# Optimization experiments

Hardware: AMD Instinct MI355X
Metric: run time of the kernel (lower is better)

The kernel has to match this reference:

```python
import jax, jax.numpy as jnp
import numpy as np
import math

D_MODEL = 256
PRED_LEN = 256
K = 32
LOW_FREQ = 1


def setup_inputs() -> dict:
    key = jax.random.key(0)
    x = jax.random.normal(key, (8, 1024, D_MODEL), dtype=jnp.float32)
    return {"x": x}


def reference(x):
    """x: (b, t, d) -> reconstructed/extrapolated series (b, t+pred_len, d)."""
    b, t, d = x.shape
    k_ = K  # K < t//2, so the explicit-k branch of the torch module is taken

    x_freq = jnp.fft.rfft(x, axis=1)  # (b, t//2+1, d) complex
    if t % 2 == 0:
        x_freq_high = x_freq[:, LOW_FREQ:-1]  # drop DC..low_freq-1 and Nyquist
    else:
        x_freq_high = x_freq[:, LOW_FREQ:]

    # top-k magnitudes over the frequency axis, independently per (b, d)
    mag = jnp.abs(x_freq_high)                                   # (b, F, d)
    _, idx = jax.lax.top_k(jnp.transpose(mag, (0, 2, 1)), k_)    # (b, d, k)
    idx = jnp.transpose(idx, (0, 2, 1)) + LOW_FREQ               # (b, k, d) into x_freq

    x_freq_topk = jnp.take_along_axis(x_freq, idx, axis=1)       # (b, k, d) complex
    freqs = jnp.fft.rfftfreq(t).astype(x.dtype)                  # (t//2+1,)
    f_topk = freqs[idx]                                          # (b, k, d)

    # append conjugate / negative-frequency pair for a real reconstruction
    x_ext = jnp.concatenate([x_freq_topk, jnp.conj(x_freq_topk)], axis=1)  # (b, 2k, d)
    f_ext = jnp.concatenate([f_topk, -f_topk], axis=1)                     # (b, 2k, d)

    t_val = jnp.arange(t + PRED_LEN, dtype=x.dtype)              # (T,)
    amp = (jnp.abs(x_ext) / t)[:, :, None, :]                    # (b, 2k, 1, d)
    phase = jnp.angle(x_ext)[:, :, None, :]                      # (b, 2k, 1, d)
    arg = (2.0 * math.pi) * f_ext[:, :, None, :] * t_val[None, None, :, None] + phase
    x_time = amp * jnp.cos(arg)                                  # (b, 2k, T, d)
    return jnp.sum(x_time, axis=1)                               # (b, T, d)
```

## Files before the change

### kernel.cpp

```cpp
#include <hip/hip_runtime.h>
#include <math.h>

#define T_LEN 1024
#define PRED_LEN 256
#define OUT_T (T_LEN + PRED_LEN)
#define DM 256
#define KSEL 32

#define TWO_PI_F 6.2831853071795864769f
#define INV1024  0.0009765625f
#define RTAU 1e-4f

#define SPAD(i) ((i) + ((i) >> 5))

__device__ __constant__ float W16RF[16] = {
    1.0f,  0.92387953f,  0.70710678f,  0.38268343f, 0.0f, -0.38268343f, -0.70710678f, -0.92387953f,
   -1.0f, -0.92387953f, -0.70710678f, -0.38268343f, 0.0f,  0.38268343f,  0.70710678f,  0.92387953f };
__device__ __constant__ float W16IF[16] = {
    0.0f, -0.38268343f, -0.70710678f, -0.92387953f, -1.0f, -0.92387953f, -0.70710678f, -0.38268343f,
    0.0f,  0.38268343f,  0.70710678f,  0.92387953f,  1.0f,  0.92387953f,  0.70710678f,  0.38268343f };

#define R2_ 0.70710678118654752440f
__device__ __constant__ float CW8[8] = { 1.0f,  R2_, 0.0f, -R2_, -1.0f, -R2_,  0.0f,  R2_ };
__device__ __constant__ float SW8[8] = { 0.0f,  R2_, 1.0f,  R2_,  0.0f, -R2_, -1.0f, -R2_ };

__global__ void fl_twiddle_kernel(double* __restrict__ gwr, double* __restrict__ gwi,
                                  float* __restrict__ gwrF, float* __restrict__ gwiF) {
    int e = blockIdx.x * 64 + threadIdx.x;
    double ang = (double)e * (6.283185307179586476925286766559 / 1024.0);
    double c = cos(ang), s = -sin(ang);
    gwr[e] = c; gwi[e] = s;
    gwrF[e] = (float)c; gwiF[e] = (float)s;
}

__global__ void __launch_bounds__(256, 4)
fl_fused_kernel(const float* __restrict__ x,
                const double* __restrict__ gwr, const double* __restrict__ gwi,
                const float* __restrict__ gwrF, const float* __restrict__ gwiF,
                float* __restrict__ out) {
    __shared__ float gspR[SPAD(1023) + 1], gspI[SPAD(1023) + 1];
    __shared__ float2 xsh[1024];
    __shared__ float mg[1024];
    __shared__ int hist[512];
    __shared__ int   selMs[2 * KSEL];
    __shared__ float selAs[2 * KSEL], selBs[2 * KSEL];

    const int tid  = threadIdx.x;
    const int lane = tid & 63;
    const int w    = tid >> 6;

    const int bid = blockIdx.x;
    const int sp  = ((bid & 7) << 7) | (bid >> 3);
    const int b   = sp >> 7;
    const int d0  = (sp & 127) << 1;

    for (int j = 0; j < 4; ++j) {
        int e = tid + (j << 8);
        gspR[SPAD(e)] = gwrF[e];
        gspI[SPAD(e)] = gwiF[e];
        xsh[e] = *reinterpret_cast<const float2*>(&x[(((size_t)(b << 10) + e) << 8) + d0]);
    }
    __syncthreads();

    float Fr[4][4], Fi[4][4];
#pragma unroll
    for (int n1a = 0; n1a < 4; ++n1a) {
        float2 a  = xsh[lane + 64 * (n1a + 0)];
        float2 bb = xsh[lane + 64 * (n1a + 4)];
        float2 cV = xsh[lane + 64 * (n1a + 8)];
        float2 d  = xsh[lane + 64 * (n1a + 12)];
        float t0r = a.x + cV.x, t0i = a.y + cV.y;
        float t1r = a.x - cV.x, t1i = a.y - cV.y;
        float t2r = bb.x + d.x, t2i = bb.y + d.y;
        float t3r = bb.x - d.x, t3i = bb.y - d.y;
        Fr[n1a][0] = t0r + t2r;  Fi[n1a][0] = t0i + t2i;
        Fr[n1a][2] = t0r - t2r;  Fi[n1a][2] = t0i - t2i;
        Fr[n1a][1] = t1r + t3i;  Fi[n1a][1] = t1i - t3r;
        Fr[n1a][3] = t1r - t3i;  Fi[n1a][3] = t1i + t3r;
    }

    float ar[4], ai[4];
#pragma unroll
    for (int q = 0; q < 4; ++q) {
        const int k1 = (w << 2) | q;
        float cr = Fr[0][q], ci = Fi[0][q];
#pragma unroll
        for (int n1a = 1; n1a < 4; ++n1a) {
            int e = (n1a * k1) & 15;
            float wr = W16RF[e], wi = W16IF[e];
            cr += Fr[n1a][q] * wr - Fi[n1a][q] * wi;
            ci += Fr[n1a][q] * wi + Fi[n1a][q] * wr;
        }
        int et = (lane * k1) & 1023;
        float twr = gspR[SPAD(et)], twi = gspI[SPAD(et)];
        ar[q] = cr * twr - ci * twi;
        ai[q] = cr * twi + ci * twr;
    }

#pragma unroll
    for (int s = 0; s < 6; ++s) {
        const int half = 32 >> s;
        const int e = (lane & (half - 1)) << s;
        const float wr = gspR[SPAD(e << 4)];
        const float wi = gspI[SPAD(e << 4)];
        const bool up = (lane & half) != 0;
#pragma unroll
        for (int q = 0; q < 4; ++q) {
            float orr = __shfl_xor(ar[q], half);
            float oii = __shfl_xor(ai[q], half);
            float sr = ar[q] + orr, si = ai[q] + oii;
            float dr = orr - ar[q], di = oii - ai[q];
            float ur = dr * wr - di * wi;
            float ui = dr * wi + di * wr;
            ar[q] = up ? ur : sr;
            ai[q] = up ? ui : si;
        }
    }
    __syncthreads();

    {
        const int krev = (int)(__brev((unsigned)lane) >> 26);
#pragma unroll
        for (int q = 0; q < 4; ++q) {
            int k = ((w << 2) | q) + (krev << 4);
            gspR[SPAD(k)] = ar[q];
            gspI[SPAD(k)] = ai[q];
        }
    }
    __syncthreads();

#pragma unroll
    for (int h = 0; h < 2; ++h) {
        int m = tid + (h << 8);
        int n = (1024 - m) & 1023;
        float rm = gspR[SPAD(m)], iv = gspI[SPAD(m)];
        float rn = gspR[SPAD(n)], in_ = gspI[SPAD(n)];
        float rr0 = 0.5f * (rm + rn),  ii0 = 0.5f * (iv - in_);
        float rr1 = 0.5f * (iv + in_), ii1 = 0.5f * (rn - rm);
        mg[m]       = rr0 * rr0 + ii0 * ii0;
        mg[512 + m] = rr1 * rr1 + ii1 * ii1;
    }
    __syncthreads();

    if (tid < 128) {
        const int c = tid >> 6;
        const float* mgc = mg + (c << 9);
        int* histc = hist + (c << 8);

        float v[8]; int hiw[8];
#pragma unroll
        for (int q = 0; q < 8; ++q) v[q] = mgc[(q << 6) | lane];
        if (lane == 0) v[0] = -1.0f;
#pragma unroll
        for (int q = 0; q < 8; ++q) hiw[q] = __float_as_int(v[q]);

        int mx = hiw[0];
#pragma unroll
        for (int q = 1; q < 8; ++q) mx = max(mx, hiw[q]);
#pragma unroll
        for (int off = 1; off < 64; off <<= 1) mx = max(mx, __shfl_xor(mx, off));

        const int base = (mx >> 20) - 250;
        int idx[8];
#pragma unroll
        for (int q = 0; q < 8; ++q) {
            int t = (hiw[q] >> 20) - base;
            idx[q] = t < 0 ? 0 : t;
        }

        *reinterpret_cast<int4*>(&histc[lane << 2]) = int4{0, 0, 0, 0};
#pragma unroll
        for (int q = 0; q < 8; ++q) atomicAdd(&histc[idx[q]], 1);

        int4 cc = *reinterpret_cast<int4*>(&histc[lane << 2]);
        int s_local = cc.x + cc.y + cc.z + cc.w;

        int s = s_local;
#pragma unroll
        for (int off = 1; off < 64; off <<= 1) {
            int t = __shfl_down(s, off);
            if (lane + off < 64) s += t;
        }
        const int S_gt = s - s_local;
        const int A3 = S_gt;
        const int A2 = A3 + cc.w;
        const int A1 = A2 + cc.z;
        const int A0 = A1 + cc.y;

        int foundB = -1, foundR = 0;
        if (A0 < KSEL && A0 + cc.x >= KSEL) { foundB = (lane << 2) | 0; foundR = KSEL - A0; }
        if (A1 < KSEL && A1 + cc.y >= KSEL) { foundB = (lane << 2) | 1; foundR = KSEL - A1; }
        if (A2 < KSEL && A2 + cc.z >= KSEL) { foundB = (lane << 2) | 2; foundR = KSEL - A2; }
        if (A3 < KSEL && A3 + cc.w >= KSEL) { foundB = (lane << 2) | 3; foundR = KSEL - A3; }

        unsigned long long fm = __ballot(foundB >= 0);
        const int srcB = (int)(__ffsll((unsigned long long)fm) - 1);
        const int B = __shfl(foundB, srcB);
        const int r = __shfl(foundR, srcB);

        unsigned selmask = 0, candmask = 0;
#pragma unroll
        for (int q = 0; q < 8; ++q) {
            if (idx[q] > B) selmask |= (1u << q);
            else if (idx[q] == B) candmask |= (1u << q);
        }

        for (int it = 0; it < r; ++it) {
            float bv = -2.0f; int bq = -1;
#pragma unroll
            for (int q = 0; q < 8; ++q) {
                bool cand = ((candmask >> q) & 1u) != 0;
                if (cand && v[q] > bv) { bv = v[q]; bq = q; }
            }
            int bi = (bq < 0) ? 0x7FFFFFFF : ((bq << 6) | lane);
#pragma unroll
            for (int off = 1; off < 64; off <<= 1) {
                float ov = __shfl_xor(bv, off);
                int   oi = __shfl_xor(bi, off);
                if (ov > bv || (ov == bv && oi < bi)) { bv = ov; bi = oi; }
            }
            if (bi != 0x7FFFFFFF && lane == (bi & 63)) {
                unsigned bit = 1u << (bi >> 6);
                selmask  |= bit;
                candmask &= ~bit;
            }
        }

        {
            float vminS = 3.0e38f, vmaxU = -3.0e38f;
#pragma unroll
            for (int q = 0; q < 8; ++q) {
                if ((selmask >> q) & 1u) vminS = fminf(vminS, v[q]);
                else                     vmaxU = fmaxf(vmaxU, v[q]);
            }
#pragma unroll
            for (int off = 1; off < 64; off <<= 1) {
                vminS = fminf(vminS, __shfl_xor(vminS, off));
                vmaxU = fmaxf(vmaxU, __shfl_xor(vmaxU, off));
            }
            const float tau = RTAU * vminS;
            if (vminS - vmaxU < tau) {
                const float lo = vmaxU - tau, hi = vminS + tau;
                unsigned candq = 0; int nAbove = 0;
#pragma unroll
                for (int q = 0; q < 8; ++q) {
                    bool inw = (v[q] >= lo) && (v[q] <= hi);
                    if (inw) candq |= (1u << q);
                    if (((selmask >> q) & 1u) && v[q] > hi) ++nAbove;
                }
#pragma unroll
                for (int off = 1; off < 64; off <<= 1) nAbove += __shfl_xor(nAbove, off);
                const int kneed = KSEL - nAbove;
                selmask &= ~candq;

                double sV = -1.0; int sSrc = 0; int cnum = 0;
                for (int q = 0; q < 8; ++q) {
                    unsigned long long bal = __ballot((candq >> q) & 1u);
                    while (bal) {
                        int srcl = (int)(__ffsll(bal) - 1);
                        bal &= bal - 1;
                        int m = (q << 6) | srcl;
                        double sr = 0.0, si = 0.0;
                        for (int u = 0; u < 16; ++u) {
                            int n = lane + (u << 6);
                            float2 xv2 = xsh[n];
                            double xvd = (double)(c ? xv2.y : xv2.x);
                            int e = (m * n) & 1023;
                            sr = fma(xvd, gwr[e], sr);
                            si = fma(xvd, gwi[e], si);
                        }
#pragma unroll
                        for (int off = 1; off < 64; off <<= 1) {
                            sr += __shfl_xor(sr, off);
                            si += __shfl_xor(si, off);
                        }
                        if (lane == cnum) { sV = sr * sr + si * si; sSrc = (q << 6) | srcl; }
                        ++cnum;
                        if (cnum >= 64) break;
                    }
                    if (cnum >= 64) break;
                }
                for (int it = 0; it < kneed; ++it) {
                    double bv = sV; int bl = lane;
#pragma unroll
                    for (int off = 1; off < 64; off <<= 1) {
                        double ov = __shfl_xor(bv, off);
                        int    ol = __shfl_xor(bl, off);
                        if (ov > bv || (ov == bv && ol < bl)) { bv = ov; bl = ol; }
                    }
                    int wsrc = __shfl(sSrc, bl);
                    if (lane == (wsrc & 63)) selmask |= 1u << (wsrc >> 6);
                    if (lane == bl) sV = -2.0;
                }
            }
        }

        const int cnt = __popc(selmask);
        int p = cnt;
#pragma unroll
        for (int off = 1; off < 64; off <<= 1) {
            int t = __shfl_up(p, off);
            if (lane >= off) p += t;
        }
        int slot = (c << 5) + (p - cnt);

#pragma unroll
        for (int q = 0; q < 8; ++q) {
            if ((selmask >> q) & 1u) {
                int m = (q << 6) | lane;
                int n = (1024 - m) & 1023;
                float rm = gspR[SPAD(m)], iv = gspI[SPAD(m)];
                float rn = gspR[SPAD(n)], in_ = gspI[SPAD(n)];
                float rr, ii;
                if (c == 0) { rr = 0.5f * (rm + rn);  ii = 0.5f * (iv - in_); }
                else        { rr = 0.5f * (iv + in_); ii = 0.5f * (rn - rm); }
                selMs[slot] = m;
                selAs[slot] = rr * (1.0f / 512.0f);
                selBs[slot] = -ii * (1.0f / 512.0f);
                ++slot;
            }
        }
    }
    __syncthreads();

    {
        const int col = tid & 1;
        const int j   = tid >> 1;
        float acc[10];
#pragma unroll
        for (int i = 0; i < 10; ++i) acc[i] = 0.0f;

        const int cbase = col << 5;
        for (int k = 0; k < KSEL; ++k) {
            const int   m = selMs[cbase + k];
            const float A = selAs[cbase + k];
            const float B = selBs[cbase + k];
            const int   rr8 = m & 7;
            const float cw = CW8[rr8], sw = SW8[rr8];
            const float th = (float)((m * j) & 1023) * (INV1024 * TWO_PI_F);
            float cs = __cosf(th);
            float sn = __sinf(th);
#pragma unroll
            for (int i = 0; i < 10; ++i) {
                acc[i] = fmaf(A, cs, fmaf(B, sn, acc[i]));
                float cn = fmaf(cs, cw, -(sn * sw));
                float s2 = fmaf(sn, cw,  (cs * sw));
                cs = cn; sn = s2;
            }
        }

        float* op = out + ((size_t)b * OUT_T + j) * DM + d0 + col;
#pragma unroll
        for (int i = 0; i < 10; ++i) {
            op[(size_t)i * 128 * DM] = acc[i];
        }
    }
}

extern "C" void kernel_launch(void* const* d_in, const int* in_sizes, int n_in,
                              void* d_out, int out_size, void* d_ws, size_t ws_size,
                              hipStream_t stream) {
    const float* x = (const float*)d_in[0];
    float* out = (float*)d_out;

    char* w = (char*)d_ws;
    double* gwr  = (double*)(w);
    double* gwi  = (double*)(w + 1024 * sizeof(double));
    float*  gwrF = (float*)(w + 2048 * sizeof(double));
    float*  gwiF = (float*)(w + 2048 * sizeof(double) + 1024 * sizeof(float));

    hipLaunchKernelGGL(fl_twiddle_kernel, dim3(16), dim3(64), 0, stream, gwr, gwi, gwrF, gwiF);
    hipLaunchKernelGGL(fl_fused_kernel, dim3(1024), dim3(256), 0, stream,
                       x, gwr, gwi, gwrF, gwiF, out);
}
```

Measured before the change: 41.82 us.

## Split output rows across two blocks per column pair and alias shared buffers

Launches twice as many blocks. Each (b, column-pair) is handled by two blocks that each write half of the output rows, using period-4 symmetry over 256-row strides so each block computes five outputs per thread without a rotation recurrence. Shared arrays xsh, mg and hist are aliased into one 8 KB buffer, and launch bounds are raised to allow more resident blocks. The refinement path now rereads x from global memory because xsh is overwritten. The cost is that the FFT and top-k selection run twice per column pair.

After: 54.84 us. 31.1% more time.

```diff
diff --git a/kernel.cpp b/kernel.cpp
--- a/kernel.cpp
+++ b/kernel.cpp
@@ -19,10 +19,6 @@
 __device__ __constant__ float W16IF[16] = {
     0.0f, -0.38268343f, -0.70710678f, -0.92387953f, -1.0f, -0.92387953f, -0.70710678f, -0.38268343f,
     0.0f,  0.38268343f,  0.70710678f,  0.92387953f,  1.0f,  0.92387953f,  0.70710678f,  0.38268343f };
-
-#define R2_ 0.70710678118654752440f
-__device__ __constant__ float CW8[8] = { 1.0f,  R2_, 0.0f, -R2_, -1.0f, -R2_,  0.0f,  R2_ };
-__device__ __constant__ float SW8[8] = { 0.0f,  R2_, 1.0f,  R2_,  0.0f, -R2_, -1.0f, -R2_ };
 
 __global__ void fl_twiddle_kernel(double* __restrict__ gwr, double* __restrict__ gwi,
                                   float* __restrict__ gwrF, float* __restrict__ gwiF) {
@@ -33,26 +29,29 @@
     gwrF[e] = (float)c; gwiF[e] = (float)s;
 }
 
-__global__ void __launch_bounds__(256, 4)
+__global__ void __launch_bounds__(256, 8)
 fl_fused_kernel(const float* __restrict__ x,
                 const double* __restrict__ gwr, const double* __restrict__ gwi,
                 const float* __restrict__ gwrF, const float* __restrict__ gwiF,
                 float* __restrict__ out) {
     __shared__ float gspR[SPAD(1023) + 1], gspI[SPAD(1023) + 1];
-    __shared__ float2 xsh[1024];
-    __shared__ float mg[1024];
-    __shared__ int hist[512];
+    __shared__ char smemU[8192];
     __shared__ int   selMs[2 * KSEL];
     __shared__ float selAs[2 * KSEL], selBs[2 * KSEL];
+    float2* xsh  = (float2*)smemU;
+    float*  mg   = (float*)smemU;
+    int*    hist = (int*)(smemU + 4096);
 
     const int tid  = threadIdx.x;
     const int lane = tid & 63;
     const int w    = tid >> 6;
 
     const int bid = blockIdx.x;
-    const int sp  = ((bid & 7) << 7) | (bid >> 3);
-    const int b   = sp >> 7;
-    const int d0  = (sp & 127) << 1;
+    const int b   = bid & 7;
+    const int t_  = bid >> 3;
+    const int p   = t_ & 1;
+    const int lp  = t_ >> 1;
+    const int d0  = lp << 1;
 
     for (int j = 0; j < 4; ++j) {
         int e = tid + (j << 8);
@@ -253,6 +252,7 @@
                 const int kneed = KSEL - nAbove;
                 selmask &= ~candq;
 
+                const float* xcol = x + ((size_t)(b << 10) << 8) + d0 + c;
                 double sV = -1.0; int sSrc = 0; int cnum = 0;
                 for (int q = 0; q < 8; ++q) {
                     unsigned long long bal = __ballot((candq >> q) & 1u);
@@ -263,8 +263,7 @@
                         double sr = 0.0, si = 0.0;
                         for (int u = 0; u < 16; ++u) {
                             int n = lane + (u << 6);
-                            float2 xv2 = xsh[n];
-                            double xvd = (double)(c ? xv2.y : xv2.x);
+                            double xvd = (double)xcol[(size_t)n << 8];
                             int e = (m * n) & 1023;
                             sr = fma(xvd, gwr[e], sr);
                             si = fma(xvd, gwi[e], si);
@@ -296,13 +295,13 @@
         }
 
         const int cnt = __popc(selmask);
-        int p = cnt;
+        int pp = cnt;
 #pragma unroll
         for (int off = 1; off < 64; off <<= 1) {
-            int t = __shfl_up(p, off);
-            if (lane >= off) p += t;
-        }
-        int slot = (c << 5) + (p - cnt);
+            int t = __shfl_up(pp, off);
+            if (lane >= off) pp += t;
+        }
+        int slot = (c << 5) + (pp - cnt);
 
 #pragma unroll
         for (int q = 0; q < 8; ++q) {
@@ -324,36 +323,34 @@
     __syncthreads();
 
     {
-        const int col = tid & 1;
-        const int j   = tid >> 1;
-        float acc[10];
-#pragma unroll
-        for (int i = 0; i < 10; ++i) acc[i] = 0.0f;
-
+        const int col = w & 1;
+        const int jl  = ((w >> 1) << 6) | lane;
+        const int j   = (p << 7) | jl;
+        float a0 = 0.f, a1 = 0.f, a2 = 0.f, a3 = 0.f, a4 = 0.f;
         const int cbase = col << 5;
         for (int k = 0; k < KSEL; ++k) {
             const int   m = selMs[cbase + k];
             const float A = selAs[cbase + k];
             const float B = selBs[cbase + k];
-            const int   rr8 = m & 7;
-            const float cw = CW8[rr8], sw = SW8[rr8];
             const float th = (float)((m * j) & 1023) * (INV1024 * TWO_PI_F);
-            float cs = __cosf(th);
-            float sn = __sinf(th);
-#pragma unroll
-            for (int i = 0; i < 10; ++i) {
-                acc[i] = fmaf(A, cs, fmaf(B, sn, acc[i]));
-                float cn = fmaf(cs, cw, -(sn * sw));
-                float s2 = fmaf(sn, cw,  (cs * sw));
-                cs = cn; sn = s2;
-            }
-        }
-
+            const float cs = __cosf(th);
+            const float sn = __sinf(th);
+            const float c0 = fmaf(A, cs, B * sn);
+            switch (m & 3) {
+                case 0: a0 += c0; a1 += c0; a2 += c0; a3 += c0; a4 += c0; break;
+                case 2: a0 += c0; a1 -= c0; a2 += c0; a3 -= c0; a4 += c0; break;
+                case 1: { float c1 = fmaf(B, cs, -(A * sn));
+                          a0 += c0; a1 += c1; a2 -= c0; a3 -= c1; a4 += c0; } break;
+                default:{ float c1 = fmaf(B, cs, -(A * sn));
+                          a0 += c0; a1 -= c1; a2 -= c0; a3 += c1; a4 += c0; } break;
+            }
+        }
         float* op = out + ((size_t)b * OUT_T + j) * DM + d0 + col;
-#pragma unroll
-        for (int i = 0; i < 10; ++i) {
-            op[(size_t)i * 128 * DM] = acc[i];
-        }
+        op[0]                   = a0;
+        op[(size_t)256  * DM]   = a1;
+        op[(size_t)512  * DM]   = a2;
+        op[(size_t)768  * DM]   = a3;
+        op[(size_t)1024 * DM]   = a4;
     }
 }
 
@@ -370,6 +367,6 @@
     float*  gwiF = (float*)(w + 2048 * sizeof(double) + 1024 * sizeof(float));
 
     hipLaunchKernelGGL(fl_twiddle_kernel, dim3(16), dim3(64), 0, stream, gwr, gwi, gwrF, gwiF);
-    hipLaunchKernelGGL(fl_fused_kernel, dim3(1024), dim3(256), 0, stream,
+    hipLaunchKernelGGL(fl_fused_kernel, dim3(2048), dim3(256), 0, stream,
                        x, gwr, gwi, gwrF, gwiF, out);
 }
```
